# Kernel tuning notes

Hardware: AMD Instinct MI355X
Metric: run time of the kernel (lower is better)

## Reference

```python
import jax, jax.numpy as jnp
import numpy as np

N_NODES = 100000
N_EDGES = 1200000
N_GRAPHS = 8
IN_DIM = 64
HID = 64
N_CLASSES = 2


def setup_inputs() -> dict:
    key = jax.random.key(0)
    ks = jax.random.split(key, 8)
    features = jax.random.normal(ks[0], (N_NODES, IN_DIM), dtype=jnp.float32)
    W1 = jax.random.normal(ks[1], (IN_DIM, HID), dtype=jnp.float32) * (1.0 / np.sqrt(IN_DIM))
    b1 = jnp.zeros((HID,), dtype=jnp.float32)
    W2 = jax.random.normal(ks[2], (HID, HID), dtype=jnp.float32) * (1.0 / np.sqrt(HID))
    b2 = jnp.zeros((HID,), dtype=jnp.float32)
    Wp = jax.random.normal(ks[3], (HID, N_CLASSES), dtype=jnp.float32) * (1.0 / np.sqrt(HID))
    bp = jnp.zeros((N_CLASSES,), dtype=jnp.float32)
    edge_src = jax.random.randint(ks[4], (N_EDGES,), 0, N_NODES, dtype=jnp.int64 if jax.config.jax_enable_x64 else jnp.int32)
    edge_dst = jax.random.randint(ks[5], (N_EDGES,), 0, N_NODES, dtype=edge_src.dtype)
    graph_id = jnp.sort(jax.random.randint(ks[6], (N_NODES,), 0, N_GRAPHS, dtype=edge_src.dtype))
    return {"features": features, "W1": W1, "b1": b1, "W2": W2, "b2": b2,
            "Wp": Wp, "bp": bp, "edge_src": edge_src, "edge_dst": edge_dst,
            "graph_id": graph_id}


def reference(features, W1, b1, W2, b2, Wp, bp, edge_src, edge_dst, graph_id):
    N = features.shape[0]
    dt = features.dtype
    ones_e = jnp.ones(edge_src.shape[0], dtype=dt)
    # DGL GraphConv norm='both': symmetric normalization with out-deg (src) / in-deg (dst)
    out_deg = jnp.clip(jax.ops.segment_sum(ones_e, edge_src, num_segments=N), 1.0)
    in_deg = jnp.clip(jax.ops.segment_sum(ones_e, edge_dst, num_segments=N), 1.0)
    src_norm = jax.lax.rsqrt(out_deg)[:, None]  # [N,1]
    dst_norm = jax.lax.rsqrt(in_deg)[:, None]   # [N,1]

    def gconv(h, W, b):
        h = h * src_norm
        msgs = h[edge_src]                                    # [E, d] gather
        agg = jax.ops.segment_sum(msgs, edge_dst, num_segments=N)  # [N, d]
        agg = agg * dst_norm
        return jax.nn.relu(agg @ W + b)

    h = gconv(features, W1, b1)   # [N, HID]
    h = gconv(h, W2, b2)          # [N, HID]

    # dgl.mean_nodes: per-graph mean pooling
    cnt = jnp.clip(jax.ops.segment_sum(jnp.ones(N, dtype=dt), graph_id, num_segments=N_GRAPHS), 1.0)
    hg = jax.ops.segment_sum(h, graph_id, num_segments=N_GRAPHS) / cnt[:, None]  # [G, HID]
    return hg @ Wp + bp
```

## Files before the change

kernel.cpp:

```cpp
#include <hip/hip_runtime.h>

#define NN 100000
#define NE 1200000
#define NG 8
#define DIM 64
#define WROW 68
#define SCAN_BS 256
#define NB ((NN + SCAN_BS - 1) / SCAN_BS)
#define COLCAP (NE + 7 * NN)

#define RANGE 8192
#define NR 13
#define GSL 28
#define SLICE4 ((NE / 4 + GSL - 1) / GSL)

__global__ __launch_bounds__(256) void hist_kernel(const int4* __restrict__ esrc4,
                                                   const int4* __restrict__ edst4,
                                                   int* __restrict__ partial) {
  __shared__ int h[RANGE];
  int job = blockIdx.x;
  int g = job % GSL;
  int r = (job / GSL) % NR;
  int dir = job / (GSL * NR);
  const int4* __restrict__ idx = dir ? edst4 : esrc4;
  int lo = r * RANGE, hi = min(lo + RANGE, NN);
  for (int i = threadIdx.x; i < RANGE / 4; i += 256) ((int4*)h)[i] = make_int4(0, 0, 0, 0);
  __syncthreads();
  int s0 = g * SLICE4, s1 = min(s0 + SLICE4, NE / 4);
  for (int i = s0 + threadIdx.x; i < s1; i += 256) {
    int4 v = idx[i];
    if (v.x >= lo && v.x < hi) atomicAdd(&h[v.x - lo], 1);
    if (v.y >= lo && v.y < hi) atomicAdd(&h[v.y - lo], 1);
    if (v.z >= lo && v.z < hi) atomicAdd(&h[v.z - lo], 1);
    if (v.w >= lo && v.w < hi) atomicAdd(&h[v.w - lo], 1);
  }
  __syncthreads();
  int4* dst = (int4*)(partial + (size_t)job * RANGE);
  int cap4 = (hi - lo) >> 2;
  for (int i = threadIdx.x; i < cap4; i += 256) dst[i] = ((int4*)h)[i];
}

__global__ void reduce_kernel(const int* __restrict__ partial, int* __restrict__ indeg,
                              float* __restrict__ snormA, float* __restrict__ dnormA, int N) {
  int t = blockIdx.x * blockDim.x + threadIdx.x;
  if (t >= 2 * N) return;
  int dir = t >= N;
  int n = dir ? t - N : t;
  int r = n >> 13, off = n & (RANGE - 1);
  const int* p = partial + (((size_t)dir * NR + r) * GSL) * RANGE + off;
  int s = 0;
#pragma unroll
  for (int g = 0; g < GSL; ++g) s += p[(size_t)g * RANGE];
  float nv = rsqrtf(fmaxf((float)s, 1.0f));
  if (dir) { indeg[n] = s; dnormA[n] = nv; }
  else snormA[n] = nv;
}

__global__ __launch_bounds__(SCAN_BS) void scan1_kernel(const int* __restrict__ indeg,
                                                        int* __restrict__ rp2,
                                                        int* __restrict__ bsum, int N) {
  __shared__ int t[SCAN_BS];
  int i = blockIdx.x * SCAN_BS + threadIdx.x;
  int v = (i < N) ? ((indeg[i] + 7) & ~7) : 0;
  t[threadIdx.x] = v;
  __syncthreads();
  for (int off = 1; off < SCAN_BS; off <<= 1) {
    int u = (threadIdx.x >= off) ? t[threadIdx.x - off] : 0;
    __syncthreads();
    t[threadIdx.x] += u;
    __syncthreads();
  }
  if (i < N) rp2[i] = t[threadIdx.x] - v;
  if (i == N - 1) rp2[N] = t[threadIdx.x];
  if (threadIdx.x == SCAN_BS - 1) bsum[blockIdx.x] = t[threadIdx.x];
}

__global__ __launch_bounds__(512) void scan2_kernel(const int* __restrict__ bsum,
                                                    int* __restrict__ boff, int nb) {
  __shared__ int t[512];
  int v = ((int)threadIdx.x < nb) ? bsum[threadIdx.x] : 0;
  t[threadIdx.x] = v;
  __syncthreads();
  for (int off = 1; off < 512; off <<= 1) {
    int u = (threadIdx.x >= off) ? t[threadIdx.x - off] : 0;
    __syncthreads();
    t[threadIdx.x] += u;
    __syncthreads();
  }
  boff[threadIdx.x] = t[threadIdx.x] - v;
}

__global__ __launch_bounds__(SCAN_BS) void scan3_kernel(int* __restrict__ rp2,
                                                        const int* __restrict__ boff, int N) {
  int i = blockIdx.x * SCAN_BS + threadIdx.x;
  if (i < N) rp2[i] += boff[blockIdx.x];
  if (i == N - 1) rp2[N] += boff[blockIdx.x];
}

__global__ void offscan_kernel(int* __restrict__ partial, const int* __restrict__ rp2, int N) {
  int n = blockIdx.x * blockDim.x + threadIdx.x;
  if (n >= N) return;
  int r = n >> 13, i = n & (RANGE - 1);
  int* p = partial + (((size_t)NR + r) * GSL) * RANGE + i;
  int running = rp2[n];
#pragma unroll
  for (int g = 0; g < GSL; ++g) {
    int tmp = p[(size_t)g * RANGE];
    p[(size_t)g * RANGE] = running;
    running += tmp;
  }
}

__global__ void colinit_kernel(int4* __restrict__ col4, int n4) {
  int i = blockIdx.x * blockDim.x + threadIdx.x;
  int st = gridDim.x * blockDim.x;
  for (; i < n4; i += st) col4[i] = make_int4(NN, NN, NN, NN);
}

__global__ __launch_bounds__(256) void fill_kernel(const int4* __restrict__ esrc4,
                                                   const int4* __restrict__ edst4,
                                                   const int* __restrict__ partial,
                                                   int* __restrict__ col) {
  __shared__ int cnt[RANGE];
  int job = blockIdx.x;
  int g = job % GSL, r = job / GSL;
  int lo = r * RANGE, hi = min(lo + RANGE, NN);
  const int* off = partial + (((size_t)NR + r) * GSL + g) * RANGE;
  for (int i = threadIdx.x; i < hi - lo; i += 256) cnt[i] = off[i];
  __syncthreads();
  int s0 = g * SLICE4, s1 = min(s0 + SLICE4, NE / 4);
  for (int i = s0 + threadIdx.x; i < s1; i += 256) {
    int4 d = edst4[i];
    int4 s = esrc4[i];
    if (d.x >= lo && d.x < hi) col[atomicAdd(&cnt[d.x - lo], 1)] = s.x;
    if (d.y >= lo && d.y < hi) col[atomicAdd(&cnt[d.y - lo], 1)] = s.y;
    if (d.z >= lo && d.z < hi) col[atomicAdd(&cnt[d.z - lo], 1)] = s.z;
    if (d.w >= lo && d.w < hi) col[atomicAdd(&cnt[d.w - lo], 1)] = s.w;
  }
}

__global__ void prescale_kernel(const float* __restrict__ f, const float* __restrict__ snormA,
                                float* __restrict__ xs, int N) {
  int i = blockIdx.x * blockDim.x + threadIdx.x;
  if (i < N * 16) {
    int n = i >> 4;
    float sn = snormA[n];
    float4 v = ((const float4*)f)[i];
    v.x *= sn; v.y *= sn; v.z *= sn; v.w *= sn;
    ((float4*)xs)[i] = v;
  }
}

template <int POOL>
__global__ __launch_bounds__(256) void gconv_kernel(
    const float* __restrict__ xs, const float* __restrict__ snormA, const float* __restrict__ dnormA,
    const int* __restrict__ rp2, const int* __restrict__ col,
    const float* __restrict__ W, const float* __restrict__ b,
    float* __restrict__ out, const int* __restrict__ gid,
    float* __restrict__ gsum, float* __restrict__ gcnt, int N) {
  __shared__ float Wt[DIM * WROW];
  __shared__ float lsum[NG * DIM];
  __shared__ float lcnt[NG];
  for (int i = threadIdx.x; i < DIM * 16; i += 256) {
    int k = i >> 4, ch = i & 15;
    *(float4*)&Wt[k * WROW + ch * 4] = *(const float4*)(W + k * DIM + ch * 4);
  }
  if (POOL) {
    for (int i = threadIdx.x; i < NG * DIM; i += 256) lsum[i] = 0.0f;
    if (threadIdx.x < NG) lcnt[threadIdx.x] = 0.0f;
  }
  __syncthreads();

  const int lane = threadIdx.x & 63;
  const int wid = threadIdx.x >> 6;
  const int g = lane >> 4;
  const int idx = lane & 15;
  const int t4 = idx << 2;
  const int gb = lane & 48;
  const float4 bb = *(const float4*)(b + t4);
  const int waveId = blockIdx.x * 4 + wid;
  const int stride4 = gridDim.x * 16;

  for (int n4 = waveId * 4; n4 < N; n4 += stride4) {
    int n = n4 + g;
    bool valid = n < N;
    int nc = valid ? n : 0;
    int base = rp2[nc];
    int end = rp2[nc + 1];
    float4 acc = make_float4(0.f, 0.f, 0.f, 0.f);
    float4 acc2 = make_float4(0.f, 0.f, 0.f, 0.f);
    for (int p = base; p < end; p += 8) {
      int4 c0 = *(const int4*)(col + p);
      int4 c1 = *(const int4*)(col + p + 4);
      float4 v0 = *(const float4*)(xs + (size_t)c0.x * DIM + t4);
      float4 v1 = *(const float4*)(xs + (size_t)c0.y * DIM + t4);
      float4 v2 = *(const float4*)(xs + (size_t)c0.z * DIM + t4);
      float4 v3 = *(const float4*)(xs + (size_t)c0.w * DIM + t4);
      float4 v4 = *(const float4*)(xs + (size_t)c1.x * DIM + t4);
      float4 v5 = *(const float4*)(xs + (size_t)c1.y * DIM + t4);
      float4 v6 = *(const float4*)(xs + (size_t)c1.z * DIM + t4);
      float4 v7 = *(const float4*)(xs + (size_t)c1.w * DIM + t4);
      acc.x += (v0.x + v1.x) + (v2.x + v3.x);
      acc.y += (v0.y + v1.y) + (v2.y + v3.y);
      acc.z += (v0.z + v1.z) + (v2.z + v3.z);
      acc.w += (v0.w + v1.w) + (v2.w + v3.w);
      acc2.x += (v4.x + v5.x) + (v6.x + v7.x);
      acc2.y += (v4.y + v5.y) + (v6.y + v7.y);
      acc2.z += (v4.z + v5.z) + (v6.z + v7.z);
      acc2.w += (v4.w + v5.w) + (v6.w + v7.w);
    }
    float dn = dnormA[nc];
    acc.x = (acc.x + acc2.x) * dn;
    acc.y = (acc.y + acc2.y) * dn;
    acc.z = (acc.z + acc2.z) * dn;
    acc.w = (acc.w + acc2.w) * dn;

    float4 r = bb;
#pragma unroll
    for (int kc = 0; kc < 16; ++kc) {
      float a0 = __shfl(acc.x, gb + kc, 64);
      float a1 = __shfl(acc.y, gb + kc, 64);
      float a2 = __shfl(acc.z, gb + kc, 64);
      float a3 = __shfl(acc.w, gb + kc, 64);
      float4 w0 = *(const float4*)(Wt + (4 * kc + 0) * WROW + t4);
      float4 w1 = *(const float4*)(Wt + (4 * kc + 1) * WROW + t4);
      float4 w2 = *(const float4*)(Wt + (4 * kc + 2) * WROW + t4);
      float4 w3 = *(const float4*)(Wt + (4 * kc + 3) * WROW + t4);
      r.x = fmaf(a0, w0.x, r.x); r.y = fmaf(a0, w0.y, r.y);
      r.z = fmaf(a0, w0.z, r.z); r.w = fmaf(a0, w0.w, r.w);
      r.x = fmaf(a1, w1.x, r.x); r.y = fmaf(a1, w1.y, r.y);
      r.z = fmaf(a1, w1.z, r.z); r.w = fmaf(a1, w1.w, r.w);
      r.x = fmaf(a2, w2.x, r.x); r.y = fmaf(a2, w2.y, r.y);
      r.z = fmaf(a2, w2.z, r.z); r.w = fmaf(a2, w2.w, r.w);
      r.x = fmaf(a3, w3.x, r.x); r.y = fmaf(a3, w3.y, r.y);
      r.z = fmaf(a3, w3.z, r.z); r.w = fmaf(a3, w3.w, r.w);
    }
    r.x = fmaxf(r.x, 0.f); r.y = fmaxf(r.y, 0.f);
    r.z = fmaxf(r.z, 0.f); r.w = fmaxf(r.w, 0.f);

    if (POOL) {
      if (valid) {
        int gi = gid[n];
        atomicAdd(&lsum[gi * DIM + t4 + 0], r.x);
        atomicAdd(&lsum[gi * DIM + t4 + 1], r.y);
        atomicAdd(&lsum[gi * DIM + t4 + 2], r.z);
        atomicAdd(&lsum[gi * DIM + t4 + 3], r.w);
        if (idx == 0) atomicAdd(&lcnt[gi], 1.0f);
      }
    } else if (valid) {
      float sn = snormA[n];
      float4 o = make_float4(r.x * sn, r.y * sn, r.z * sn, r.w * sn);
      *(float4*)(out + (size_t)n * DIM + t4) = o;
    }
  }

  if (POOL) {
    __syncthreads();
    for (int i = threadIdx.x; i < NG * DIM; i += 256) atomicAdd(&gsum[i], lsum[i]);
    if (threadIdx.x < NG) atomicAdd(&gcnt[threadIdx.x], lcnt[threadIdx.x]);
  }
}

__global__ void final_kernel(const float* __restrict__ gsum, const float* __restrict__ gcnt,
                             const float* __restrict__ Wp, const float* __restrict__ bp,
                             float* __restrict__ out) {
  int lane = threadIdx.x;
#pragma unroll
  for (int g = 0; g < NG; ++g) {
    float inv = 1.0f / fmaxf(gcnt[g], 1.0f);
    float hv = gsum[g * DIM + lane] * inv;
#pragma unroll
    for (int c = 0; c < 2; ++c) {
      float p = hv * Wp[lane * 2 + c];
      for (int off = 32; off; off >>= 1) p += __shfl_down(p, off, 64);
      if (lane == 0) out[g * 2 + c] = p + bp[c];
    }
  }
}

extern "C" void kernel_launch(void* const* d_in, const int* in_sizes, int n_in,
                              void* d_out, int out_size, void* d_ws, size_t ws_size,
                              hipStream_t stream) {
  const float* features = (const float*)d_in[0];
  const float* W1 = (const float*)d_in[1];
  const float* b1 = (const float*)d_in[2];
  const float* W2 = (const float*)d_in[3];
  const float* b2 = (const float*)d_in[4];
  const float* Wp = (const float*)d_in[5];
  const float* bp = (const float*)d_in[6];
  const int* esrc = (const int*)d_in[7];
  const int* edst = (const int*)d_in[8];
  const int* gid = (const int*)d_in[9];
  float* out = (float*)d_out;

  const int N = NN;

  float* base = (float*)d_ws;
  size_t off = 0;
  auto alloc = [&](size_t nwords) { size_t r = off; off = (off + nwords + 15) & ~(size_t)15; return r; };

  float* gsum = base + alloc(NG * DIM);
  float* gcnt = base + alloc(NG);
  size_t zeroWords = off;
  int* indeg  = (int*)(base + alloc(N));
  float* snormA = base + alloc(N);
  float* dnormA = base + alloc(N);
  int* rp2   = (int*)(base + alloc(N + 1));
  int* bsum  = (int*)(base + alloc(512));
  int* boff  = (int*)(base + alloc(512));
  int* col   = (int*)(base + alloc(COLCAP));
  float* xs  = base + alloc((size_t)(N + 1) * DIM);
  float* B   = base + alloc((size_t)(N + 1) * DIM);
  int* partial = (int*)xs;

  hipMemsetAsync(d_ws, 0, zeroWords * sizeof(float), stream);
  hipMemsetAsync(xs + (size_t)N * DIM, 0, DIM * sizeof(float), stream);
  hipMemsetAsync(B + (size_t)N * DIM, 0, DIM * sizeof(float), stream);

  hist_kernel<<<2 * NR * GSL, 256, 0, stream>>>((const int4*)esrc, (const int4*)edst, partial);
  reduce_kernel<<<(2 * N + 255) / 256, 256, 0, stream>>>(partial, indeg, snormA, dnormA, N);

  scan1_kernel<<<NB, SCAN_BS, 0, stream>>>(indeg, rp2, bsum, N);
  scan2_kernel<<<1, 512, 0, stream>>>(bsum, boff, NB);
  scan3_kernel<<<NB, SCAN_BS, 0, stream>>>(rp2, boff, N);

  offscan_kernel<<<(NR * RANGE + 255) / 256, 256, 0, stream>>>(partial, rp2, N);
  colinit_kernel<<<(COLCAP / 4 + 255) / 256, 256, 0, stream>>>((int4*)col, COLCAP / 4);
  fill_kernel<<<NR * GSL, 256, 0, stream>>>((const int4*)esrc, (const int4*)edst, partial, col);

  prescale_kernel<<<(N * 16 + 255) / 256, 256, 0, stream>>>(features, snormA, xs, N);

  gconv_kernel<0><<<2048, 256, 0, stream>>>(xs, snormA, dnormA, rp2, col, W1, b1,
                                            B, gid, gsum, gcnt, N);
  gconv_kernel<1><<<2048, 256, 0, stream>>>(B, snormA, dnormA, rp2, col, W2, b2,
                                            nullptr, gid, gsum, gcnt, N);

  final_kernel<<<1, 64, 0, stream>>>(gsum, gcnt, Wp, bp, out);
}
```

Before: 249.8 us.

## Split fused gconv into separate gather and dense-transform kernels

Splits each graph-convolution kernel into a gather-only kernel that writes the normalized aggregate to a buffer and a separate matmul/ReLU/pool kernel that reads it back. The gather kernel carries no LDS weight tile and declares higher occupancy in its launch bounds, so more waves can hide the random-gather latency. In exchange it adds an extra round-trip of the N×64 intermediate through memory and two more kernel launches. Buffers are ping-ponged between xs and B, and the transform kernel writes in place.

```diff
diff --git a/kernel.cpp b/kernel.cpp
--- a/kernel.cpp
+++ b/kernel.cpp
@@ -151,33 +151,14 @@
   }
 }
 
-template <int POOL>
-__global__ __launch_bounds__(256) void gconv_kernel(
-    const float* __restrict__ xs, const float* __restrict__ snormA, const float* __restrict__ dnormA,
+__global__ __launch_bounds__(256, 8) void gather_kernel(
+    const float* __restrict__ xs, const float* __restrict__ dnormA,
     const int* __restrict__ rp2, const int* __restrict__ col,
-    const float* __restrict__ W, const float* __restrict__ b,
-    float* __restrict__ out, const int* __restrict__ gid,
-    float* __restrict__ gsum, float* __restrict__ gcnt, int N) {
-  __shared__ float Wt[DIM * WROW];
-  __shared__ float lsum[NG * DIM];
-  __shared__ float lcnt[NG];
-  for (int i = threadIdx.x; i < DIM * 16; i += 256) {
-    int k = i >> 4, ch = i & 15;
-    *(float4*)&Wt[k * WROW + ch * 4] = *(const float4*)(W + k * DIM + ch * 4);
-  }
-  if (POOL) {
-    for (int i = threadIdx.x; i < NG * DIM; i += 256) lsum[i] = 0.0f;
-    if (threadIdx.x < NG) lcnt[threadIdx.x] = 0.0f;
-  }
-  __syncthreads();
-
+    float* __restrict__ y, int N) {
   const int lane = threadIdx.x & 63;
   const int wid = threadIdx.x >> 6;
   const int g = lane >> 4;
-  const int idx = lane & 15;
-  const int t4 = idx << 2;
-  const int gb = lane & 48;
-  const float4 bb = *(const float4*)(b + t4);
+  const int t4 = (lane & 15) << 2;
   const int waveId = blockIdx.x * 4 + wid;
   const int stride4 = gridDim.x * 16;
 
@@ -209,19 +190,58 @@
       acc2.z += (v4.z + v5.z) + (v6.z + v7.z);
       acc2.w += (v4.w + v5.w) + (v6.w + v7.w);
     }
-    float dn = dnormA[nc];
-    acc.x = (acc.x + acc2.x) * dn;
-    acc.y = (acc.y + acc2.y) * dn;
-    acc.z = (acc.z + acc2.z) * dn;
-    acc.w = (acc.w + acc2.w) * dn;
+    if (valid) {
+      float dn = dnormA[n];
+      acc.x = (acc.x + acc2.x) * dn;
+      acc.y = (acc.y + acc2.y) * dn;
+      acc.z = (acc.z + acc2.z) * dn;
+      acc.w = (acc.w + acc2.w) * dn;
+      *(float4*)(y + (size_t)n * DIM + t4) = acc;
+    }
+  }
+}
+
+template <int POOL>
+__global__ __launch_bounds__(256) void mlp2_kernel(
+    float* __restrict__ Y, const float* __restrict__ snormA,
+    const float* __restrict__ W, const float* __restrict__ b,
+    const int* __restrict__ gid, float* __restrict__ gsum, float* __restrict__ gcnt, int N) {
+  __shared__ float Wt[DIM * WROW];
+  __shared__ float lsum[NG * DIM];
+  __shared__ float lcnt[NG];
+  for (int i = threadIdx.x; i < DIM * 16; i += 256) {
+    int k = i >> 4, ch = i & 15;
+    *(float4*)&Wt[k * WROW + ch * 4] = *(const float4*)(W + k * DIM + ch * 4);
+  }
+  if (POOL) {
+    for (int i = threadIdx.x; i < NG * DIM; i += 256) lsum[i] = 0.0f;
+    if (threadIdx.x < NG) lcnt[threadIdx.x] = 0.0f;
+  }
+  __syncthreads();
+
+  const int lane = threadIdx.x & 63;
+  const int wid = threadIdx.x >> 6;
+  const int g = lane >> 4;
+  const int idx = lane & 15;
+  const int t4 = idx << 2;
+  const int gb = lane & 48;
+  const float4 bb = *(const float4*)(b + t4);
+  const int waveId = blockIdx.x * 4 + wid;
+  const int stride4 = gridDim.x * 16;
+
+  for (int n4 = waveId * 4; n4 < N; n4 += stride4) {
+    int n = n4 + g;
+    bool valid = n < N;
+    int nc = valid ? n : 0;
+    float4 a = *(const float4*)(Y + (size_t)nc * DIM + t4);
 
     float4 r = bb;
 #pragma unroll
     for (int kc = 0; kc < 16; ++kc) {
-      float a0 = __shfl(acc.x, gb + kc, 64);
-      float a1 = __shfl(acc.y, gb + kc, 64);
-      float a2 = __shfl(acc.z, gb + kc, 64);
-      float a3 = __shfl(acc.w, gb + kc, 64);
+      float a0 = __shfl(a.x, gb + kc, 64);
+      float a1 = __shfl(a.y, gb + kc, 64);
+      float a2 = __shfl(a.z, gb + kc, 64);
+      float a3 = __shfl(a.w, gb + kc, 64);
       float4 w0 = *(const float4*)(Wt + (4 * kc + 0) * WROW + t4);
       float4 w1 = *(const float4*)(Wt + (4 * kc + 1) * WROW + t4);
       float4 w2 = *(const float4*)(Wt + (4 * kc + 2) * WROW + t4);
@@ -250,7 +270,7 @@
     } else if (valid) {
       float sn = snormA[n];
       float4 o = make_float4(r.x * sn, r.y * sn, r.z * sn, r.w * sn);
-      *(float4*)(out + (size_t)n * DIM + t4) = o;
+      *(float4*)(Y + (size_t)n * DIM + t4) = o;
     }
   }
 
@@ -330,10 +350,10 @@
 
   prescale_kernel<<<(N * 16 + 255) / 256, 256, 0, stream>>>(features, snormA, xs, N);
 
-  gconv_kernel<0><<<2048, 256, 0, stream>>>(xs, snormA, dnormA, rp2, col, W1, b1,
-                                            B, gid, gsum, gcnt, N);
-  gconv_kernel<1><<<2048, 256, 0, stream>>>(B, snormA, dnormA, rp2, col, W2, b2,
-                                            nullptr, gid, gsum, gcnt, N);
+  gather_kernel<<<2048, 256, 0, stream>>>(xs, dnormA, rp2, col, B, N);
+  mlp2_kernel<0><<<2048, 256, 0, stream>>>(B, snormA, W1, b1, gid, gsum, gcnt, N);
+  gather_kernel<<<2048, 256, 0, stream>>>(B, dnormA, rp2, col, xs, N);
+  mlp2_kernel<1><<<2048, 256, 0, stream>>>(xs, snormA, W2, b2, gid, gsum, gcnt, N);
 
   final_kernel<<<1, 64, 0, stream>>>(gsum, gcnt, Wp, bp, out);
 }
```

Result: slower. 309.1 us (+23.7%).
